# Kernel optimization log

Hardware: AMD Instinct MI355X
Metric: run time of the kernel (lower is better)

Reference implementation:

```python
import jax, jax.numpy as jnp
import numpy as np

B, C, H, W = 8, 256, 64, 64
NH = 8
CM = 2048
EPS = 1e-5


def setup_inputs() -> dict:
    key = jax.random.key(0)
    ks = jax.random.split(key, 16)
    n = lambda k, s: (jax.random.normal(k, s, dtype=jnp.float32) * 0.02)
    return {
        'x': jax.random.normal(ks[0], (B, C, H, W), dtype=jnp.float32),
        'Wqkv': n(ks[1], (C, 3 * C)), 'bqkv': n(ks[2], (3 * C,)),
        'dw_w': n(ks[3], (C, 1, 3, 3)), 'dw_b': n(ks[4], (C,)),
        'Wproj': n(ks[5], (C, C)), 'bproj': n(ks[6], (C,)),
        'bn1_g': jnp.ones((C,), jnp.float32), 'bn1_b': jnp.zeros((C,), jnp.float32),
        'bn1_m': n(ks[7], (C,)), 'bn1_v': jax.random.uniform(ks[8], (C,), dtype=jnp.float32) + 0.5,
        'alpha1': jnp.ones((1,), jnp.float32),
        'Wfc1': n(ks[9], (C, CM)), 'bfc1': n(ks[10], (CM,)),
        'Wfc2': n(ks[11], (CM, C)), 'bfc2': n(ks[12], (C,)),
        'bn2_g': jnp.ones((C,), jnp.float32), 'bn2_b': jnp.zeros((C,), jnp.float32),
        'bn2_m': n(ks[13], (C,)), 'bn2_v': jax.random.uniform(ks[14], (C,), dtype=jnp.float32) + 0.5,
        'alpha2': jnp.ones((1,), jnp.float32),
    }


def _repbn(x, g, b, m, v, alpha):
    # eval-mode RepBN: BatchNorm1d with running stats over channel dim + alpha*x
    bn = (x - m) * jax.lax.rsqrt(v + EPS) * g + b
    return bn + alpha * x


def reference(x, Wqkv, bqkv, dw_w, dw_b, Wproj, bproj,
              bn1_g, bn1_b, bn1_m, bn1_v, alpha1,
              Wfc1, bfc1, Wfc2, bfc2,
              bn2_g, bn2_b, bn2_m, bn2_v, alpha2):
    b, c, h, w = x.shape
    n = h * w
    hd = c // NH
    scale = hd ** (-0.5)
    t = x.reshape(b, c, n).transpose(0, 2, 1)  # [B,N,C]

    # --- SimplifiedLinearAttention ---
    qkv = (t @ Wqkv + bqkv).reshape(b, n, 3, NH, hd).transpose(2, 0, 3, 1, 4)
    q, k, v = qkv[0], qkv[1], qkv[2]          # [B,H,N,hd]
    q = jax.nn.relu(q) * scale
    k = jax.nn.relu(k)
    ctx = jnp.einsum('bhnd,bhne->bhde', k, v)  # [B,H,hd,hd] small context
    out = jnp.einsum('bhnd,bhde->bhne', q, ctx)
    out = out.transpose(0, 2, 1, 3).reshape(b, n, c)
    img = out.transpose(0, 2, 1).reshape(b, c, h, w)
    img = jax.lax.conv_general_dilated(img, dw_w, (1, 1), 'SAME',
                                       feature_group_count=c)
    img = img + dw_b[None, :, None, None]
    out = img.reshape(b, c, n).transpose(0, 2, 1)
    out = out @ Wproj + bproj

    # residual + RepBN (eval branch of LinearNorm)
    t = _repbn(t + out, bn1_g, bn1_b, bn1_m, bn1_v, alpha1)

    # FFN (exact GELU as nn.GELU default)
    ff = jax.nn.gelu(t @ Wfc1 + bfc1, approximate=False) @ Wfc2 + bfc2
    t = _repbn(t + ff, bn2_g, bn2_b, bn2_m, bn2_v, alpha2)

    return t.transpose(0, 2, 1).reshape(b, c, h, w)
```

## Files before the change

### kernel.cpp

```cpp
#include <hip/hip_runtime.h>
#include <hip/hip_bf16.h>
#include <math.h>

constexpr int B_ = 8, C_ = 256, H_ = 64, W_ = 64;
constexpr int N_ = H_ * W_;
constexpr int NH_ = 8;
constexpr int CM_ = 2048;
constexpr int M_ = B_ * N_;
constexpr float EPS_ = 1e-5f;

typedef __bf16 bf16_t;
typedef bf16_t bf16x4 __attribute__((ext_vector_type(4)));
typedef bf16_t bf16x8 __attribute__((ext_vector_type(8)));
typedef float f32x4 __attribute__((ext_vector_type(4)));

__device__ inline bf16_t f2b(float f) {
    __hip_bfloat16 h = __float2bfloat16(f);
    return *reinterpret_cast<bf16_t*>(&h);
}
__device__ inline float b2f(bf16_t b) {
    unsigned short u = *reinterpret_cast<unsigned short*>(&b);
    unsigned int x = (unsigned int)u << 16;
    return *reinterpret_cast<float*>(&x);
}
__device__ inline float gelu_ap(float y) {
    float u = y * (0.7978845608f + 0.0356774081f * y * y);
    float e = __expf(2.0f * u);
    return y - y * __builtin_amdgcn_rcpf(e + 1.0f);
}

#define GLOAD_LDS16(gptr, lptr)                                                     \
    __builtin_amdgcn_global_load_lds(                                               \
        (const __attribute__((address_space(1))) void*)(gptr),                      \
        (__attribute__((address_space(3))) void*)(lptr), 16, 0, 0)

__global__ __launch_bounds__(256)
void prep(const float* __restrict__ x, bf16_t* __restrict__ t_b,
          const float* __restrict__ Wqkv, bf16_t* __restrict__ WqkvT,
          const float* __restrict__ Wproj, bf16_t* __restrict__ WprojT,
          const float* __restrict__ Wfc1, bf16_t* __restrict__ Wfc1T,
          const float* __restrict__ Wfc2, bf16_t* __restrict__ Wfc2T) {
    __shared__ float tile[32][33];
    int id = blockIdx.x;
    int tx = threadIdx.x, ty = threadIdx.y;

    const float* src;
    bf16_t* dst;
    int K, N, k0, n0;
    size_t soff, doff;

    if (id < 8192) {
        int b = id >> 10, rem = id & 1023;
        int nn = (rem & 127) * 32, cc = (rem >> 7) * 32;
        src = x; dst = t_b; K = 0; N = 0;
#pragma unroll
        for (int i = ty; i < 32; i += 8)
            tile[i][tx] = x[(size_t)b * C_ * N_ + (size_t)(cc + i) * N_ + nn + tx];
        __syncthreads();
#pragma unroll
        for (int i = ty; i < 32; i += 8)
            t_b[(size_t)b * N_ * C_ + (size_t)(nn + i) * C_ + cc + tx] = f2b(tile[tx][i]);
        return;
    } else if (id < 8384) {
        int idw = id - 8192; K = C_; N = 768;
        n0 = (idw % 24) * 32; k0 = (idw / 24) * 32;
        src = Wqkv; dst = WqkvT;
    } else if (id < 8448) {
        int idw = id - 8384; K = C_; N = C_;
        n0 = (idw & 7) * 32; k0 = (idw >> 3) * 32;
        src = Wproj; dst = WprojT;
    } else if (id < 8960) {
        int idw = id - 8448; K = C_; N = CM_;
        n0 = (idw & 63) * 32; k0 = (idw >> 6) * 32;
        src = Wfc1; dst = Wfc1T;
    } else {
        int idw = id - 8960; K = CM_; N = C_;
        n0 = (idw & 7) * 32; k0 = (idw >> 3) * 32;
        src = Wfc2; dst = Wfc2T;
    }
#pragma unroll
    for (int i = ty; i < 32; i += 8)
        tile[i][tx] = src[(size_t)(k0 + i) * N + n0 + tx];
    __syncthreads();
#pragma unroll
    for (int i = ty; i < 32; i += 8)
        dst[(size_t)(n0 + i) * K + k0 + tx] = f2b(tile[tx][i]);
}

template <int EPI>
__global__ __launch_bounds__(256)
void gemm_swp(const bf16_t* __restrict__ Wt, const bf16_t* __restrict__ Act,
              const float* __restrict__ bias, bf16_t* __restrict__ Cb,
              int M, int N, int K,
              const bf16_t* __restrict__ tres_b,
              const float* __restrict__ g, const float* __restrict__ bb,
              const float* __restrict__ mm, const float* __restrict__ vv,
              const float* __restrict__ alpha) {
    __shared__ bf16x8 ldsv[4096];
    char* lds = (char*)ldsv;

    int tid  = threadIdx.x;
    int lane = tid & 63;
    int w    = tid >> 6;
    int wi   = w >> 1, wj = w & 1;

    int nwg = gridDim.x * gridDim.y;
    int bid = blockIdx.y * gridDim.x + blockIdx.x;
    int swz = (bid & 7) * (nwg >> 3) + (bid >> 3);
    int bx = swz % gridDim.x, by = swz / gridDim.x;
    int bch = bx * 128, bm = by * 128;

    int rowl = lane & 15, kq = lane >> 4;

    const bf16_t* wbase = Wt  + (size_t)(bch + (w >> 1) * 32) * K;
    (void)wbase;

#define STAGE_SWP(k0, p)                                                             \
    {                                                                                \
        _Pragma("unroll")                                                            \
        for (int j = 0; j < 4; ++j) {                                                \
            int jj = w * 4 + j;                                                      \
            int msub = jj >> 1, kh = jj & 1;                                         \
            const bf16_t* gw = Wt + ((size_t)(bch + msub * 16 + rowl) * K + (k0) +   \
                                     kh * 32 + kq * 8);                              \
            GLOAD_LDS16(gw, lds + (p) * 32768 + jj * 1024);                          \
            const bf16_t* ga = Act + ((size_t)(bm + msub * 16 + rowl) * K + (k0) +   \
                                      kh * 32 + kq * 8);                             \
            GLOAD_LDS16(ga, lds + (p) * 32768 + 16384 + jj * 1024);                  \
        }                                                                            \
    }

    f32x4 acc[4][4] = {};
    int T = K >> 6;

    STAGE_SWP(0, 0);
    __syncthreads();

    for (int t = 0; t < T; ++t) {
        int p = t & 1;
        if (t + 1 < T) STAGE_SWP((t + 1) << 6, p ^ 1);
#pragma unroll
        for (int ks = 0; ks < 2; ++ks) {
            bf16x8 wf[4], af[4];
#pragma unroll
            for (int i = 0; i < 4; ++i) wf[i] = ldsv[p * 2048 + ((wi * 4 + i) * 2 + ks) * 64 + lane];
#pragma unroll
            for (int j = 0; j < 4; ++j) af[j] = ldsv[p * 2048 + 1024 + ((wj * 4 + j) * 2 + ks) * 64 + lane];
#pragma unroll
            for (int i = 0; i < 4; ++i)
#pragma unroll
                for (int j = 0; j < 4; ++j)
                    acc[i][j] = __builtin_amdgcn_mfma_f32_16x16x32_bf16(wf[i], af[j], acc[i][j], 0, 0, 0);
        }
        if (t + 1 < T) __syncthreads();
    }

    float alpha_v = (EPI == 1) ? alpha[0] : 0.f;
#pragma unroll
    for (int i = 0; i < 4; ++i) {
        int ch = bch + wi * 64 + i * 16 + (lane >> 4) * 4;
        f32x4 b4 = *(const f32x4*)(bias + ch);
        f32x4 rs4, B4, m4;
        if (EPI == 1) {
            f32x4 g4 = *(const f32x4*)(g + ch);
            f32x4 v4 = *(const f32x4*)(vv + ch);
            B4 = *(const f32x4*)(bb + ch);
            m4 = *(const f32x4*)(mm + ch);
#pragma unroll
            for (int r = 0; r < 4; ++r) rs4[r] = rsqrtf(v4[r] + EPS_) * g4[r];
        }
#pragma unroll
        for (int j = 0; j < 4; ++j) {
            int m = bm + wj * 64 + j * 16 + (lane & 15);
            f32x4 a = acc[i][j];
            bf16_t ob[4];
            if (EPI == 4) {
#pragma unroll
                for (int r = 0; r < 4; ++r) ob[r] = f2b(a[r] + b4[r]);
            } else if (EPI == 2) {
#pragma unroll
                for (int r = 0; r < 4; ++r) ob[r] = f2b(gelu_ap(a[r] + b4[r]));
            } else {
                bf16x4 t4 = *(const bf16x4*)(tres_b + (size_t)m * N + ch);
#pragma unroll
                for (int r = 0; r < 4; ++r) {
                    float z = b2f(t4[r]) + a[r] + b4[r];
                    ob[r] = f2b((z - m4[r]) * rs4[r] + B4[r] + alpha_v * z);
                }
            }
            *(bf16x4*)(Cb + (size_t)m * N + ch) = *(bf16x4*)ob;
        }
    }
}

__global__ __launch_bounds__(256)
void gemm_bf16(const bf16_t* __restrict__ A, const bf16_t* __restrict__ Bt,
               const float* __restrict__ bias,
               float* __restrict__ Cf,
               int M, int N, int K,
               const bf16_t* __restrict__ tres_b,
               const float* __restrict__ g, const float* __restrict__ bb,
               const float* __restrict__ mm, const float* __restrict__ vv,
               const float* __restrict__ alpha) {
    __shared__ bf16x8 ldsv[4096];
    char* lds = (char*)ldsv;

    int tid  = threadIdx.x;
    int lane = tid & 63;
    int w    = tid >> 6;
    int wm   = w >> 1, wn = w & 1;

    int nwg = gridDim.x * gridDim.y;
    int bid = blockIdx.y * gridDim.x + blockIdx.x;
    int swz = (bid & 7) * (nwg >> 3) + (bid >> 3);
    int bx = swz % gridDim.x, by = swz / gridDim.x;
    int brow = by * 128, bcol = bx * 128;

    int rowl = lane & 15, kq = lane >> 4;

#define STAGE_NSW(k0, p)                                                             \
    {                                                                                \
        _Pragma("unroll")                                                            \
        for (int j = 0; j < 4; ++j) {                                                \
            int jj = w * 4 + j;                                                      \
            int msub = jj >> 1, kh = jj & 1;                                         \
            const bf16_t* ga = A + ((size_t)(brow + msub * 16 + rowl) * K + (k0) +   \
                                    kh * 32 + kq * 8);                               \
            GLOAD_LDS16(ga, lds + (p) * 32768 + jj * 1024);                          \
            const bf16_t* gb = Bt + ((size_t)(bcol + msub * 16 + rowl) * K + (k0) +  \
                                     kh * 32 + kq * 8);                              \
            GLOAD_LDS16(gb, lds + (p) * 32768 + 16384 + jj * 1024);                  \
        }                                                                            \
    }

    f32x4 acc[4][4] = {};
    int T = K >> 6;

    STAGE_NSW(0, 0);
    __syncthreads();

    for (int t = 0; t < T; ++t) {
        int p = t & 1;
        if (t + 1 < T) STAGE_NSW((t + 1) << 6, p ^ 1);
#pragma unroll
        for (int ks = 0; ks < 2; ++ks) {
            bf16x8 af[4], bfr[4];
#pragma unroll
            for (int m = 0; m < 4; ++m) af[m] = ldsv[p * 2048 + ((wm * 4 + m) * 2 + ks) * 64 + lane];
#pragma unroll
            for (int n = 0; n < 4; ++n) bfr[n] = ldsv[p * 2048 + 1024 + ((wn * 4 + n) * 2 + ks) * 64 + lane];
#pragma unroll
            for (int m = 0; m < 4; ++m)
#pragma unroll
                for (int n = 0; n < 4; ++n)
                    acc[m][n] = __builtin_amdgcn_mfma_f32_16x16x32_bf16(af[m], bfr[n], acc[m][n], 0, 0, 0);
        }
        if (t + 1 < T) __syncthreads();
    }

    float alpha_v = alpha[0];
#pragma unroll
    for (int m = 0; m < 4; ++m) {
        int mbase = brow + wm * 64 + m * 16 + (lane >> 4) * 4;
        int bi = mbase >> 12, ni = mbase & (N_ - 1);
#pragma unroll
        for (int n = 0; n < 4; ++n) {
            int col = bcol + wn * 64 + n * 16 + (lane & 15);
            float bv = bias[col];
            float rs = rsqrtf(vv[col] + EPS_) * g[col];
            float bbv = bb[col], mv = mm[col];
            f32x4 o4;
#pragma unroll
            for (int r = 0; r < 4; ++r) {
                float z = b2f(tres_b[(size_t)(mbase + r) * C_ + col]) + acc[m][n][r] + bv;
                o4[r] = (z - mv) * rs + bbv + alpha_v * z;
            }
            *(f32x4*)(Cf + ((size_t)bi * C_ + col) * N_ + ni) = o4;
        }
    }
}

__global__ void transpose_b(const bf16_t* __restrict__ in_, bf16_t* __restrict__ outb) {
    __shared__ float tile[32][33];
    int b  = blockIdx.z;
    int n0 = blockIdx.x * 32;
    int c0 = blockIdx.y * 32;
    int tx = threadIdx.x, ty = threadIdx.y;
#pragma unroll
    for (int i = ty; i < 32; i += 8)
        tile[i][tx] = b2f(in_[(size_t)b * C_ * N_ + (size_t)(c0 + i) * N_ + n0 + tx]);
    __syncthreads();
#pragma unroll
    for (int i = ty; i < 32; i += 8)
        outb[(size_t)b * N_ * C_ + (size_t)(n0 + i) * C_ + c0 + tx] = f2b(tile[tx][i]);
}

__global__ void ctx_partial(const bf16_t* __restrict__ qkv, float* __restrict__ ctxp) {
    __shared__ float kb[64][40];
    __shared__ float vb[64][40];
    int seg = blockIdx.x;
    int bh  = blockIdx.y;
    int b = bh >> 3, h = bh & 7;
    int tid = threadIdx.x;
    int d  = tid >> 3;
    int e0 = (tid & 7) * 4;
    int lrow = tid >> 2, lcol = (tid & 3) * 8;
    float acc[4] = {0.f, 0.f, 0.f, 0.f};
    const size_t base = (size_t)b * N_ * 768 + h * 32;
    for (int n0 = seg * 512; n0 < seg * 512 + 512; n0 += 64) {
        size_t ra = base + (size_t)(n0 + lrow) * 768 + lcol;
        bf16x8 kv8 = *(const bf16x8*)(qkv + ra + 256);
        bf16x8 vv8 = *(const bf16x8*)(qkv + ra + 512);
#pragma unroll
        for (int j = 0; j < 8; ++j) {
            kb[lrow][lcol + j] = b2f(kv8[j]);
            vb[lrow][lcol + j] = b2f(vv8[j]);
        }
        __syncthreads();
#pragma unroll
        for (int nl = 0; nl < 64; ++nl) {
            float kv = fmaxf(kb[nl][d], 0.f);
#pragma unroll
            for (int j = 0; j < 4; ++j)
                acc[j] = fmaf(kv, vb[nl][e0 + j], acc[j]);
        }
        __syncthreads();
    }
    float* o = ctxp + ((size_t)seg * 64 + bh) * 1024 + d * 32 + e0;
#pragma unroll
    for (int j = 0; j < 4; ++j) o[j] = acc[j];
}

__global__ void ctx_reduce(const float* __restrict__ ctxp, float* __restrict__ ctx) {
    int idx = blockIdx.x * 256 + threadIdx.x;
    float s = 0.f;
#pragma unroll
    for (int seg = 0; seg < 8; ++seg) s += ctxp[(size_t)seg * 65536 + idx];
    ctx[idx] = s;
}

__global__ void attn_out(const bf16_t* __restrict__ qkv, const float* __restrict__ ctx,
                         bf16_t* __restrict__ img) {
    __shared__ float qb[64][33];
    __shared__ float cs[32][32];
    int n0 = blockIdx.x * 64;
    int bh = blockIdx.y;
    int b = bh >> 3, h = bh & 7;
    int tid = threadIdx.x;
    const float scale = 0.17677669529663687f;
    {
        float4 vv = ((const float4*)(ctx + (size_t)bh * 1024))[tid];
        ((float4*)&cs[0][0])[tid] = vv;
    }
    const size_t base = (size_t)b * N_ * 768 + h * 32;
    int lrow = tid >> 2, lcol = (tid & 3) * 8;
    {
        bf16x8 q8 = *(const bf16x8*)(qkv + base + (size_t)(n0 + lrow) * 768 + lcol);
#pragma unroll
        for (int j = 0; j < 8; ++j)
            qb[lrow][lcol + j] = fmaxf(b2f(q8[j]), 0.f) * scale;
    }
    __syncthreads();
    int nl = tid & 63, ebase = tid >> 6;
    bf16_t* outp = img + ((size_t)b * C_ + h * 32) * N_ + n0 + nl;
#pragma unroll
    for (int p = 0; p < 8; ++p) {
        int e = ebase + p * 4;
        float s = 0.f;
#pragma unroll
        for (int dd = 0; dd < 32; ++dd)
            s = fmaf(qb[nl][dd], cs[dd][e], s);
        outp[(size_t)e * N_] = f2b(s);
    }
}

__global__ __launch_bounds__(256)
void dwconv3x3(const bf16_t* __restrict__ img, const float* __restrict__ w,
               const float* __restrict__ bias, bf16_t* __restrict__ out) {
    __shared__ float sp[64][65];
    int bc = blockIdx.x;
    int c  = bc & 255;
    int tid = threadIdx.x;
    const bf16_t* ip = img + (size_t)bc * N_;
#pragma unroll
    for (int l = 0; l < 2; ++l) {
        int flat = (tid + l * 256) * 8;
        int row = flat >> 6, col = flat & 63;
        bf16x8 v8 = *(const bf16x8*)(ip + flat);
#pragma unroll
        for (int j = 0; j < 8; ++j) sp[row][col + j] = b2f(v8[j]);
    }
    float wv[9];
#pragma unroll
    for (int j = 0; j < 9; ++j) wv[j] = w[c * 9 + j];
    float bv = bias[c];
    __syncthreads();

    int y = tid >> 2, x0 = (tid & 3) * 16;
    float o[16];
#pragma unroll
    for (int i = 0; i < 16; ++i) o[i] = bv;
#pragma unroll
    for (int dy = -1; dy <= 1; ++dy) {
        int yy = y + dy;
        if (yy < 0 || yy > 63) continue;
#pragma unroll
        for (int dx = -1; dx <= 1; ++dx) {
            float wgt = wv[(dy + 1) * 3 + dx + 1];
#pragma unroll
            for (int i = 0; i < 16; ++i) {
                int xx = x0 + i + dx;
                float val = (xx < 0 || xx > 63) ? 0.f : sp[yy][xx];
                o[i] = fmaf(wgt, val, o[i]);
            }
        }
    }
    bf16_t ob[16];
#pragma unroll
    for (int i = 0; i < 16; ++i) ob[i] = f2b(o[i]);
    *(bf16x8*)(out + (size_t)bc * N_ + y * 64 + x0)     = *(bf16x8*)&ob[0];
    *(bf16x8*)(out + (size_t)bc * N_ + y * 64 + x0 + 8) = *(bf16x8*)&ob[8];
}

extern "C" void kernel_launch(void* const* d_in, const int* in_sizes, int n_in,
                              void* d_out, int out_size, void* d_ws, size_t ws_size,
                              hipStream_t stream) {
    const float* x     = (const float*)d_in[0];
    const float* Wqkv  = (const float*)d_in[1];
    const float* bqkv  = (const float*)d_in[2];
    const float* dw_w  = (const float*)d_in[3];
    const float* dw_b  = (const float*)d_in[4];
    const float* Wproj = (const float*)d_in[5];
    const float* bproj = (const float*)d_in[6];
    const float* bn1_g = (const float*)d_in[7];
    const float* bn1_b = (const float*)d_in[8];
    const float* bn1_m = (const float*)d_in[9];
    const float* bn1_v = (const float*)d_in[10];
    const float* alpha1= (const float*)d_in[11];
    const float* Wfc1  = (const float*)d_in[12];
    const float* bfc1  = (const float*)d_in[13];
    const float* Wfc2  = (const float*)d_in[14];
    const float* bfc2  = (const float*)d_in[15];
    const float* bn2_g = (const float*)d_in[16];
    const float* bn2_b = (const float*)d_in[17];
    const float* bn2_m = (const float*)d_in[18];
    const float* bn2_v = (const float*)d_in[19];
    const float* alpha2= (const float*)d_in[20];
    float* out = (float*)d_out;

    char* ws = (char*)d_ws;
    bf16_t* t_b2    = (bf16_t*)(ws);
    bf16_t* WqkvT   = (bf16_t*)(ws + 16777216);
    bf16_t* WprojT  = (bf16_t*)(ws + 17170432);
    bf16_t* Wfc1T   = (bf16_t*)(ws + 17301504);
    bf16_t* Wfc2T   = (bf16_t*)(ws + 18350080);
    float*  ctxp    = (float*)(ws + 19398656);
    float*  ctx     = (float*)(ws + 21495808);
    bf16_t* t_b     = (bf16_t*)(ws + 21757952);
    bf16_t* qkv_b   = (bf16_t*)(ws + 38535168);
    bf16_t* img_b   = (bf16_t*)(ws + 88866816);
    bf16_t* conv_b  = (bf16_t*)(ws + 105644032);
    bf16_t* convT_b = (bf16_t*)(ws + 122421248);
    bf16_t* hidden  = (bf16_t*)(ws + 21757952);

    prep<<<9472, dim3(32, 8), 0, stream>>>(x, t_b, Wqkv, WqkvT, Wproj, WprojT,
                                           Wfc1, Wfc1T, Wfc2, Wfc2T);

    gemm_swp<4><<<dim3(768 / 128, M_ / 128), 256, 0, stream>>>(
        WqkvT, t_b, bqkv, qkv_b, M_, 768, C_,
        nullptr, nullptr, nullptr, nullptr, nullptr, nullptr);

    ctx_partial<<<dim3(8, B_ * NH_), 256, 0, stream>>>(qkv_b, ctxp);
    ctx_reduce<<<256, 256, 0, stream>>>(ctxp, ctx);

    attn_out<<<dim3(N_ / 64, B_ * NH_), 256, 0, stream>>>(qkv_b, ctx, img_b);

    dwconv3x3<<<B_ * C_, 256, 0, stream>>>(img_b, dw_w, dw_b, conv_b);

    transpose_b<<<dim3(N_ / 32, C_ / 32, B_), dim3(32, 8), 0, stream>>>(conv_b, convT_b);

    gemm_swp<1><<<dim3(C_ / 128, M_ / 128), 256, 0, stream>>>(
        WprojT, convT_b, bproj, t_b2, M_, C_, C_,
        t_b, bn1_g, bn1_b, bn1_m, bn1_v, alpha1);

    gemm_swp<2><<<dim3(CM_ / 128, M_ / 128), 256, 0, stream>>>(
        Wfc1T, t_b2, bfc1, hidden, M_, CM_, C_,
        nullptr, nullptr, nullptr, nullptr, nullptr, nullptr);

    gemm_bf16<<<dim3(C_ / 128, M_ / 128), 256, 0, stream>>>(
        hidden, Wfc2T, bfc2, out, M_, C_, CM_,
        t_b2, bn2_g, bn2_b, bn2_m, bn2_v, alpha2);
}
```

Measured before the change: 332.2 us.

## Fuse FFN fc1+GELU+fc2+RepBN into one kernel keeping hidden in LDS

```diff
diff --git a/kernel.cpp b/kernel.cpp
--- a/kernel.cpp
+++ b/kernel.cpp
@@ -22,6 +22,12 @@
     unsigned short u = *reinterpret_cast<unsigned short*>(&b);
     unsigned int x = (unsigned int)u << 16;
     return *reinterpret_cast<float*>(&x);
+}
+__device__ inline unsigned pk2(float lo, float hi) {
+    bf16_t l = f2b(lo), h = f2b(hi);
+    unsigned short ls = *reinterpret_cast<unsigned short*>(&l);
+    unsigned short hs = *reinterpret_cast<unsigned short*>(&h);
+    return ((unsigned)hs << 16) | (unsigned)ls;
 }
 __device__ inline float gelu_ap(float y) {
     float u = y * (0.7978845608f + 0.0356774081f * y * y);
@@ -47,12 +53,10 @@
     const float* src;
     bf16_t* dst;
     int K, N, k0, n0;
-    size_t soff, doff;
 
     if (id < 8192) {
         int b = id >> 10, rem = id & 1023;
         int nn = (rem & 127) * 32, cc = (rem >> 7) * 32;
-        src = x; dst = t_b; K = 0; N = 0;
 #pragma unroll
         for (int i = ty; i < 32; i += 8)
             tile[i][tx] = x[(size_t)b * C_ * N_ + (size_t)(cc + i) * N_ + nn + tx];
@@ -112,9 +116,6 @@
 
     int rowl = lane & 15, kq = lane >> 4;
 
-    const bf16_t* wbase = Wt  + (size_t)(bch + (w >> 1) * 32) * K;
-    (void)wbase;
-
 #define STAGE_SWP(k0, p)                                                             \
     {                                                                                \
         _Pragma("unroll")                                                            \
@@ -177,9 +178,6 @@
             if (EPI == 4) {
 #pragma unroll
                 for (int r = 0; r < 4; ++r) ob[r] = f2b(a[r] + b4[r]);
-            } else if (EPI == 2) {
-#pragma unroll
-                for (int r = 0; r < 4; ++r) ob[r] = f2b(gelu_ap(a[r] + b4[r]));
             } else {
                 bf16x4 t4 = *(const bf16x4*)(tres_b + (size_t)m * N + ch);
 #pragma unroll
@@ -193,89 +191,100 @@
     }
 }
 
-__global__ __launch_bounds__(256)
-void gemm_bf16(const bf16_t* __restrict__ A, const bf16_t* __restrict__ Bt,
-               const float* __restrict__ bias,
-               float* __restrict__ Cf,
-               int M, int N, int K,
-               const bf16_t* __restrict__ tres_b,
+__global__ __launch_bounds__(512, 2)
+void ffn_fused(const bf16_t* __restrict__ Act, const bf16_t* __restrict__ W1t,
+               const bf16_t* __restrict__ W2t,
+               const float* __restrict__ bfc1, const float* __restrict__ bfc2,
                const float* __restrict__ g, const float* __restrict__ bb,
                const float* __restrict__ mm, const float* __restrict__ vv,
-               const float* __restrict__ alpha) {
-    __shared__ bf16x8 ldsv[4096];
-    char* lds = (char*)ldsv;
-
-    int tid  = threadIdx.x;
-    int lane = tid & 63;
-    int w    = tid >> 6;
-    int wm   = w >> 1, wn = w & 1;
-
-    int nwg = gridDim.x * gridDim.y;
-    int bid = blockIdx.y * gridDim.x + blockIdx.x;
-    int swz = (bid & 7) * (nwg >> 3) + (bid >> 3);
-    int bx = swz % gridDim.x, by = swz / gridDim.x;
-    int brow = by * 128, bcol = bx * 128;
-
-    int rowl = lane & 15, kq = lane >> 4;
-
-#define STAGE_NSW(k0, p)                                                             \
-    {                                                                                \
-        _Pragma("unroll")                                                            \
-        for (int j = 0; j < 4; ++j) {                                                \
-            int jj = w * 4 + j;                                                      \
-            int msub = jj >> 1, kh = jj & 1;                                         \
-            const bf16_t* ga = A + ((size_t)(brow + msub * 16 + rowl) * K + (k0) +   \
-                                    kh * 32 + kq * 8);                               \
-            GLOAD_LDS16(ga, lds + (p) * 32768 + jj * 1024);                          \
-            const bf16_t* gb = Bt + ((size_t)(bcol + msub * 16 + rowl) * K + (k0) +  \
-                                     kh * 32 + kq * 8);                              \
-            GLOAD_LDS16(gb, lds + (p) * 32768 + 16384 + jj * 1024);                  \
-        }                                                                            \
-    }
-
-    f32x4 acc[4][4] = {};
-    int T = K >> 6;
-
-    STAGE_NSW(0, 0);
-    __syncthreads();
-
-    for (int t = 0; t < T; ++t) {
-        int p = t & 1;
-        if (t + 1 < T) STAGE_NSW((t + 1) << 6, p ^ 1);
-#pragma unroll
-        for (int ks = 0; ks < 2; ++ks) {
-            bf16x8 af[4], bfr[4];
-#pragma unroll
-            for (int m = 0; m < 4; ++m) af[m] = ldsv[p * 2048 + ((wm * 4 + m) * 2 + ks) * 64 + lane];
-#pragma unroll
-            for (int n = 0; n < 4; ++n) bfr[n] = ldsv[p * 2048 + 1024 + ((wn * 4 + n) * 2 + ks) * 64 + lane];
-#pragma unroll
-            for (int m = 0; m < 4; ++m)
-#pragma unroll
-                for (int n = 0; n < 4; ++n)
-                    acc[m][n] = __builtin_amdgcn_mfma_f32_16x16x32_bf16(af[m], bfr[n], acc[m][n], 0, 0, 0);
-        }
-        if (t + 1 < T) __syncthreads();
+               const float* __restrict__ alpha, float* __restrict__ out) {
+    __shared__ char lds[49152];
+    bf16x8* ldsA = (bf16x8*)lds;
+    bf16x8* ldsH = (bf16x8*)(lds + 32768);
+
+    const int tid = threadIdx.x;
+    const int lane = tid & 63;
+    const int w = tid >> 6;
+    const int l15 = lane & 15;
+    const int kq = lane >> 4;
+    const int m0 = blockIdx.x * 64;
+
+#pragma unroll
+    for (int j = 0; j < 4; ++j) {
+        int jj = w * 4 + j;
+        int mblk = jj >> 3, ks = jj & 7;
+        const bf16_t* src = Act + (size_t)(m0 + mblk * 16 + l15) * 256 + ks * 32 + kq * 8;
+        GLOAD_LDS16(src, lds + jj * 1024);
+    }
+    __syncthreads();
+
+    f32x4 acc2[2][4] = {};
+
+    const int hrow = w * 16 + l15;
+    const int ks2w = w >> 1;
+    const int lane2 = l15 + (((2 * w + (kq >> 1)) & 3) << 4);
+    const int hwoff = (kq & 1) << 3;
+    const int chb = w * 32;
+
+    for (int c = 0; c < 16; ++c) {
+        bf16x8 w1f[8];
+#pragma unroll
+        for (int ks = 0; ks < 8; ++ks)
+            w1f[ks] = *(const bf16x8*)(W1t + (size_t)(c * 128 + hrow) * 256 + ks * 32 + kq * 8);
+        f32x4 acc1[4] = {};
+#pragma unroll
+        for (int ks = 0; ks < 8; ++ks)
+#pragma unroll
+            for (int mblk = 0; mblk < 4; ++mblk)
+                acc1[mblk] = __builtin_amdgcn_mfma_f32_16x16x32_bf16(
+                    w1f[ks], ldsA[(mblk * 8 + ks) * 64 + lane], acc1[mblk], 0, 0, 0);
+
+        f32x4 b1 = *(const f32x4*)(bfc1 + c * 128 + w * 16 + kq * 4);
+#pragma unroll
+        for (int mblk = 0; mblk < 4; ++mblk) {
+            unsigned lo = pk2(gelu_ap(acc1[mblk][0] + b1[0]), gelu_ap(acc1[mblk][1] + b1[1]));
+            unsigned hi = pk2(gelu_ap(acc1[mblk][2] + b1[2]), gelu_ap(acc1[mblk][3] + b1[3]));
+            char* dst = lds + 32768 + (size_t)((mblk * 4 + ks2w) * 64 + lane2) * 16 + hwoff;
+            *(unsigned*)dst = lo;
+            *(unsigned*)(dst + 4) = hi;
+        }
+        __syncthreads();
+
+        bf16x8 w2f[2][4];
+#pragma unroll
+        for (int cf = 0; cf < 2; ++cf)
+#pragma unroll
+            for (int ks2 = 0; ks2 < 4; ++ks2)
+                w2f[cf][ks2] = *(const bf16x8*)(W2t + (size_t)(chb + cf * 16 + l15) * 2048 + c * 128 + ks2 * 32 + kq * 8);
+#pragma unroll
+        for (int mblk = 0; mblk < 4; ++mblk)
+#pragma unroll
+            for (int ks2 = 0; ks2 < 4; ++ks2) {
+                bf16x8 hf = ldsH[(mblk * 4 + ks2) * 64 + lane];
+                acc2[0][mblk] = __builtin_amdgcn_mfma_f32_16x16x32_bf16(hf, w2f[0][ks2], acc2[0][mblk], 0, 0, 0);
+                acc2[1][mblk] = __builtin_amdgcn_mfma_f32_16x16x32_bf16(hf, w2f[1][ks2], acc2[1][mblk], 0, 0, 0);
+            }
+        __syncthreads();
     }
 
     float alpha_v = alpha[0];
 #pragma unroll
-    for (int m = 0; m < 4; ++m) {
-        int mbase = brow + wm * 64 + m * 16 + (lane >> 4) * 4;
-        int bi = mbase >> 12, ni = mbase & (N_ - 1);
-#pragma unroll
-        for (int n = 0; n < 4; ++n) {
-            int col = bcol + wn * 64 + n * 16 + (lane & 15);
-            float bv = bias[col];
-            float rs = rsqrtf(vv[col] + EPS_) * g[col];
-            float bbv = bb[col], mv = mm[col];
+    for (int cf = 0; cf < 2; ++cf) {
+        int ch = chb + cf * 16 + l15;
+        float b2v = bfc2[ch];
+        float rs = rsqrtf(vv[ch] + EPS_) * g[ch];
+        float bbv = bb[ch], mv = mm[ch];
+#pragma unroll
+        for (int mblk = 0; mblk < 4; ++mblk) {
+            int mbase = m0 + mblk * 16 + kq * 4;
             f32x4 o4;
 #pragma unroll
             for (int r = 0; r < 4; ++r) {
-                float z = b2f(tres_b[(size_t)(mbase + r) * C_ + col]) + acc[m][n][r] + bv;
+                float z = b2f(Act[(size_t)(mbase + r) * 256 + ch]) + acc2[cf][mblk][r] + b2v;
                 o4[r] = (z - mv) * rs + bbv + alpha_v * z;
             }
-            *(f32x4*)(Cf + ((size_t)bi * C_ + col) * N_ + ni) = o4;
+            int bi = mbase >> 12, ni = mbase & (N_ - 1);
+            *(f32x4*)(out + ((size_t)bi * C_ + ch) * N_ + ni) = o4;
         }
     }
 }
@@ -461,7 +470,6 @@
     bf16_t* img_b   = (bf16_t*)(ws + 88866816);
     bf16_t* conv_b  = (bf16_t*)(ws + 105644032);
     bf16_t* convT_b = (bf16_t*)(ws + 122421248);
-    bf16_t* hidden  = (bf16_t*)(ws + 21757952);
 
     prep<<<9472, dim3(32, 8), 0, stream>>>(x, t_b, Wqkv, WqkvT, Wproj, WprojT,
                                            Wfc1, Wfc1T, Wfc2, Wfc2T);
@@ -483,11 +491,7 @@
         WprojT, convT_b, bproj, t_b2, M_, C_, C_,
         t_b, bn1_g, bn1_b, bn1_m, bn1_v, alpha1);
 
-    gemm_swp<2><<<dim3(CM_ / 128, M_ / 128), 256, 0, stream>>>(
-        Wfc1T, t_b2, bfc1, hidden, M_, CM_, C_,
-        nullptr, nullptr, nullptr, nullptr, nullptr, nullptr);
-
-    gemm_bf16<<<dim3(C_ / 128, M_ / 128), 256, 0, stream>>>(
-        hidden, Wfc2T, bfc2, out, M_, C_, CM_,
-        t_b2, bn2_g, bn2_b, bn2_m, bn2_v, alpha2);
-}
+    ffn_fused<<<M_ / 64, 512, 0, stream>>>(
+        t_b2, Wfc1T, Wfc2T, bfc1, bfc2,
+        bn2_g, bn2_b, bn2_m, bn2_v, alpha2, out);
+}
```

Result: faster. 303.7 us (-8.6%).
